# Kernel optimization log

Measured on AMD Instinct MI355X. Metric: run time of the kernel, lower is better.

Reference implementation:

```python
import jax, jax.numpy as jnp
import numpy as np

N, E, C, NB, NE, G = 20000, 320000, 64, 8, 4, 16
L2 = 9          # (max_ell+1)^2 with max_ell=2
RMAX = 5.0
HID = 16        # nonlinear readout hidden width


def setup_inputs():
    key = jax.random.key(0)
    ks = jax.random.split(key, 16)
    positions = jax.random.uniform(ks[0], (N, 3), dtype=jnp.float32) * 3.0
    elems = jax.random.randint(ks[1], (N,), 0, NE)
    node_attrs = jax.nn.one_hot(elems, NE, dtype=jnp.float32)
    edge_index = jax.random.randint(ks[2], (2, E), 0, N)
    batch = jnp.sort(jax.random.randint(ks[3], (N,), 0, G))
    shifts = jnp.zeros((E, 3), jnp.float32)
    atomic_energies = jnp.array([-1.0, -2.0, -3.0, -4.0], jnp.float32)
    sc = lambda k, shp, fan: jax.random.normal(k, shp, jnp.float32) / np.sqrt(fan).astype(np.float32)
    W_embed = sc(ks[4], (NE, C), NE)
    W_up = sc(ks[5], (2, C, C), C)
    W1 = sc(ks[6], (2, NB, 64), NB)
    W2 = sc(ks[7], (2, 64, C), 64)
    W_out = sc(ks[8], (2, C, C), C)
    W_skip = sc(ks[9], (2, NE, C), NE)
    w_read0 = sc(ks[10], (C,), C)
    W_r1 = sc(ks[11], (C, HID), C)
    w_r2 = sc(ks[12], (HID,), HID)
    return dict(positions=positions, node_attrs=node_attrs, shifts=shifts,
                atomic_energies=atomic_energies, W_embed=W_embed, W_up=W_up,
                W1=W1, W2=W2, W_out=W_out, W_skip=W_skip, w_read0=w_read0,
                W_r1=W_r1, w_r2=w_r2, edge_index=edge_index, batch=batch)


def _sph_harm_l2(u):
    # component-normalized real spherical harmonics up to l=2 on unit vectors
    x, y, z = u[:, 0], u[:, 1], u[:, 2]
    s3, s5, s15 = jnp.sqrt(3.0), jnp.sqrt(5.0), jnp.sqrt(15.0)
    return jnp.stack([jnp.ones_like(x),
                      s3 * x, s3 * y, s3 * z,
                      s15 * x * y, s15 * y * z, 0.5 * s5 * (3.0 * z * z - 1.0),
                      s15 * x * z, 0.5 * s15 * (x * x - y * y)], axis=-1)


def _radial(r):
    # Bessel radial basis with polynomial cutoff (p=6)
    n = jnp.arange(1, NB + 1, dtype=jnp.float32)
    rb = jnp.sqrt(2.0 / RMAX) * jnp.sin(n * jnp.pi * r[:, None] / RMAX) / r[:, None]
    u = r / RMAX
    fc = 1.0 - 28.0 * u**6 + 48.0 * u**7 - 21.0 * u**8
    fc = jnp.where(u < 1.0, fc, 0.0)
    return rb * fc[:, None]


def _energy_contributions(positions, node_attrs, shifts, atomic_energies,
                          W_embed, W_up, W1, W2, W_out, W_skip,
                          w_read0, W_r1, w_r2, edge_index, batch):
    snd, rcv = edge_index[0], edge_index[1]
    vec = positions[snd] - positions[rcv] + shifts                  # [E,3]
    r = jnp.sqrt(jnp.sum(vec * vec, axis=-1) + 1e-12)               # [E]
    Y = _sph_harm_l2(vec / r[:, None])                              # [E,L2]
    ef = _radial(r)                                                 # [E,NB]
    # E0: per-element reference energies, summed per graph
    e0 = jax.ops.segment_sum(node_attrs @ atomic_energies, batch, num_segments=G)
    h0 = node_attrs @ W_embed                                       # [N,C] scalar feats
    h = jnp.zeros((positions.shape[0], L2, C), h0.dtype).at[:, 0, :].set(h0)
    readouts = [lambda s: s @ w_read0,
                lambda s: jax.nn.silu(s @ W_r1) @ w_r2]             # linear / nonlinear
    energies = [e0]
    for i in range(2):
        hu = jnp.einsum('nlc,cd->nld', h, W_up[i])                  # channel mix
        R = jax.nn.silu(ef @ W1[i]) @ W2[i]                         # radial MLP [E,C]
        s = jnp.einsum('elc,el->ec', hu[snd], Y)                    # equivariant contraction
        m = Y[:, :, None] * (R * s)[:, None, :]                     # [E,L2,C] messages
        agg = jax.ops.segment_sum(m, rcv, num_segments=positions.shape[0])
        h = jnp.einsum('nlc,cd->nld', agg, W_out[i])
        h = h.at[:, 0, :].add(node_attrs @ W_skip[i])               # scalar skip connection
        node_en = readouts[i](h[:, 0, :])                           # [N]
        energies.append(jax.ops.segment_sum(node_en, batch, num_segments=G))
    return jnp.stack(energies, axis=-1)                             # [G, num_interactions+1]


def reference(positions, node_attrs, shifts, atomic_energies, W_embed, W_up,
              W1, W2, W_out, W_skip, w_read0, W_r1, w_r2, edge_index, batch):
    contributions = _energy_contributions(positions, node_attrs, shifts,
        atomic_energies, W_embed, W_up, W1, W2, W_out, W_skip,
        w_read0, W_r1, w_r2, edge_index, batch)
    total_energy = jnp.sum(contributions, axis=-1)                  # [G]
    forces = -jax.grad(lambda p: jnp.sum(_energy_contributions(p, node_attrs,
        shifts, atomic_energies, W_embed, W_up, W1, W2, W_out, W_skip,
        w_read0, W_r1, w_r2, edge_index, batch)))(positions)        # [N,3]
    return total_energy, contributions, forces
```

## Files before the change

kernel.cpp:

```cpp
#include <hip/hip_runtime.h>
#include <cmath>

constexpr int N_  = 20000;
constexpr int E_  = 320000;
constexpr int NE_ = 4;
constexpr int G_  = 16;
constexpr int CAP = 96;
constexpr int TAB = 4096;
constexpr float RMAXF = 5.0f;
constexpr float PI_F  = 3.14159265358979323846f;
constexpr float S3  = 1.7320508075688772f;
constexpr float S5  = 2.2360679774997896f;
constexpr float S15 = 3.8729833462074170f;
constexpr float KC_ = 0.6324555320336759f;

typedef unsigned short u16;
typedef unsigned int   u32;
typedef _Float16 f16;
typedef _Float16 f16x2 __attribute__((ext_vector_type(2)));

#define DEV static __device__ __forceinline__

__device__ float g_fallback[110000000];

DEV float sigmoidf_(float x){ return 1.0f/(1.0f+__expf(-x)); }

DEV float b2f(u16 u){ return __uint_as_float(((u32)u)<<16); }
DEV u16  f2b(float f){
  u32 x = __float_as_uint(f);
  return (u16)((x + 0x7FFFu + ((x>>16)&1u)) >> 16);
}
DEV u16  f2h(float f){ union{f16 h; u16 u;} v; v.h=(f16)f; return v.u; }
DEV float h2f(u16 u){ union{u16 u2; f16 h;} v; v.u2=u; return (float)v.h; }

DEV f16x2 u2h(u32 x){ union{u32 u; f16x2 h;} v; v.u=x; return v.h; }
DEV u32 h2u(f16x2 h){ union{u32 u; f16x2 h;} v; v.h=h; return v.u; }
DEV u32 pkh(float a, float b){ f16x2 h; h.x=(f16)a; h.y=(f16)b; return h2u(h); }

DEV void ld4(const float* __restrict__ p, float* d){
  float4 a = ((const float4*)p)[0];
  d[0]=a.x; d[1]=a.y; d[2]=a.z; d[3]=a.w;
}
DEV void ld4b(const u16* __restrict__ p, float* d){
  ushort4 a = *(const ushort4*)p;
  d[0]=b2f(a.x); d[1]=b2f(a.y); d[2]=b2f(a.z); d[3]=b2f(a.w);
}
DEV void ld4h(const u16* __restrict__ p, float* d){
  ushort4 a = *(const ushort4*)p;
  d[0]=h2f(a.x); d[1]=h2f(a.y); d[2]=h2f(a.z); d[3]=h2f(a.w);
}
DEV void st8b(u16* p, const float* d){
  uint4 v;
  v.x = (u32)f2b(d[0]) | ((u32)f2b(d[1])<<16);
  v.y = (u32)f2b(d[2]) | ((u32)f2b(d[3])<<16);
  v.z = (u32)f2b(d[4]) | ((u32)f2b(d[5])<<16);
  v.w = (u32)f2b(d[6]) | ((u32)f2b(d[7])<<16);
  *(uint4*)p = v;
}
DEV void st8h(u16* p, const float* d){
  uint4 v;
  v.x = pkh(d[0],d[1]); v.y = pkh(d[2],d[3]);
  v.z = pkh(d[4],d[5]); v.w = pkh(d[6],d[7]);
  *(uint4*)p = v;
}

__global__ void k_csr(const int* __restrict__ ei, int* __restrict__ cntR, int* __restrict__ cntS,
                      int* __restrict__ listR, int* __restrict__ listS){
  int e = blockIdx.x*256 + threadIdx.x;
  int s = ei[e], r = ei[E_+e];
  int p = atomicAdd(&cntR[r], 1); if (p < CAP) listR[r*CAP+p] = e;
  int q = atomicAdd(&cntS[s], 1); if (q < CAP) listS[s*CAP+q] = e;
}

__global__ void k_pre(const float* __restrict__ Wout0, const float* __restrict__ Wup1,
                      const float* __restrict__ Wskip0, const float* __restrict__ wread0,
                      float* __restrict__ WA, float* __restrict__ sa,
                      float* __restrict__ va, float* __restrict__ sv){
  int t = threadIdx.x;
  for (int idx=t; idx<4096; idx+=256){
    int c = idx>>6, d = idx&63;
    float acc=0.f;
    for (int m=0;m<64;++m) acc += Wout0[c*64+m]*Wup1[m*64+d];
    WA[idx]=acc;
  }
  {
    int k = t>>6, d = t&63;
    float acc=0.f;
    for (int m=0;m<64;++m) acc += Wskip0[k*64+m]*Wup1[m*64+d];
    sa[t]=acc;
  }
  if (t<64){
    float acc=0.f;
    for (int d=0;d<64;++d) acc += Wout0[t*64+d]*wread0[d];
    va[t]=acc;
  }
  if (t<4){
    float acc=0.f;
    for (int d=0;d<64;++d) acc += Wskip0[t*64+d]*wread0[d];
    sv[t]=acc;
  }
}

__global__ __launch_bounds__(256, 2)
void k_rtab(const float* __restrict__ W1g, const float* __restrict__ W2g,
            u16* __restrict__ tab){
  __shared__ float sW1[1024];
  __shared__ u32   sW2h[4096];
  __shared__ u32   sAh[32*36];
  int t = threadIdx.x;
  for (int i=t;i<1024;i+=256) sW1[i]=W1g[i];
  for (int i=t;i<4096;i+=256){
    int L = i>>11, rem = i&2047, kp = rem>>6, c = rem&63;
    sW2h[i] = pkh(W2g[L*4096 + (2*kp)*64 + c], W2g[L*4096 + (2*kp+1)*64 + c]);
  }
  __syncthreads();
  int wid=t>>6, lane=t&63, q=lane>>3, j=lane&7, c0=j*8;
  int slot = wid*8 + q;
  int knot = blockIdx.x*32 + slot;
  bool valid = (knot <= TAB);
  float rad = fmaxf((float)knot * (RMAXF/(float)TAB), 1e-6f);
  float inv = 1.0f/rad;
  float tt = rad*(1.0f/RMAXF);
  float fc = 0.0f, dfc = 0.0f;
  if (tt < 1.0f){
    float t2=tt*tt, t4=t2*t2, t5=t4*tt, t6=t5*tt, t7=t6*tt, t8=t7*tt;
    fc  = 1.0f - 28.0f*t6 + 48.0f*t7 - 21.0f*t8;
    dfc = (-168.0f*t5 + 336.0f*t6 - 168.0f*t7)*(1.0f/RMAXF);
  }
  float th = rad*(PI_F/RMAXF);
  float s1 = __sinf(th), c1 = __cosf(th);
  float base = KC_*inv*fc;
  float efv[8], gfv[8];
  {
    float sb = s1, cb = c1;
    #pragma unroll
    for (int b=0;b<8;++b){
      efv[b] = base*sb;
      float wb_ = (float)(b+1)*(PI_F/RMAXF);
      float rb  = KC_*sb*inv;
      float drb = KC_*(wb_*cb - sb*inv)*inv;
      gfv[b] = drb*fc + rb*dfc;
      float sn = sb*c1 + cb*s1;
      cb = cb*c1 - sb*s1;
      sb = sn;
    }
  }
  u32* myAh = sAh + slot*36;
  for (int L=0; L<2; ++L){
    const float* w1 = sW1 + L*512;
    const u32*  w2h = sW2h + L*2048;
    float zz[8]={0,0,0,0,0,0,0,0};
    float wgv[8]={0,0,0,0,0,0,0,0};
    #pragma unroll 4
    for (int b=0;b<8;++b){
      float efb = efv[b], gfb = gfv[b];
      const float4* w=(const float4*)(w1 + b*64 + c0);
      float4 wa=w[0], wb=w[1];
      zz[0]+=efb*wa.x; zz[1]+=efb*wa.y; zz[2]+=efb*wa.z; zz[3]+=efb*wa.w;
      zz[4]+=efb*wb.x; zz[5]+=efb*wb.y; zz[6]+=efb*wb.z; zz[7]+=efb*wb.w;
      wgv[0]+=gfb*wa.x; wgv[1]+=gfb*wa.y; wgv[2]+=gfb*wa.z; wgv[3]+=gfb*wa.w;
      wgv[4]+=gfb*wb.x; wgv[5]+=gfb*wb.y; wgv[6]+=gfb*wb.z; wgv[7]+=gfb*wb.w;
    }
    float a[8], dv[8];
    #pragma unroll
    for (int i=0;i<8;++i){
      float sg = sigmoidf_(zz[i]);
      a[i]  = zz[i]*sg;
      float sp = sg*(1.0f + zz[i]*(1.0f - sg));
      dv[i] = wgv[i]*sp;
    }
    {
      uint4 av;
      av.x = pkh(a[0],a[1]); av.y = pkh(a[2],a[3]);
      av.z = pkh(a[4],a[5]); av.w = pkh(a[6],a[7]);
      *(uint4*)(myAh + 4*j) = av;
    }
    {
      float r0=0.f,r1=0.f,r2=0.f,r3=0.f,r4=0.f,r5=0.f,r6=0.f,r7=0.f;
      #pragma unroll 2
      for (int kp4=0; kp4<8; ++kp4){
        uint4 dq = *(const uint4*)(myAh + 4*kp4);
        #pragma unroll
        for (int i=0;i<4;++i){
          u32 du = (i==0)?dq.x:(i==1)?dq.y:(i==2)?dq.z:dq.w;
          f16x2 dh = u2h(du);
          const u32* wrow = w2h + (4*kp4+i)*64 + c0;
          uint4 w0 = *(const uint4*)(wrow);
          uint4 w1v = *(const uint4*)(wrow+4);
          r0 = __builtin_amdgcn_fdot2(dh, u2h(w0.x),  r0, false);
          r1 = __builtin_amdgcn_fdot2(dh, u2h(w0.y),  r1, false);
          r2 = __builtin_amdgcn_fdot2(dh, u2h(w0.z),  r2, false);
          r3 = __builtin_amdgcn_fdot2(dh, u2h(w0.w),  r3, false);
          r4 = __builtin_amdgcn_fdot2(dh, u2h(w1v.x), r4, false);
          r5 = __builtin_amdgcn_fdot2(dh, u2h(w1v.y), r5, false);
          r6 = __builtin_amdgcn_fdot2(dh, u2h(w1v.z), r6, false);
          r7 = __builtin_amdgcn_fdot2(dh, u2h(w1v.w), r7, false);
        }
      }
      float racc[8] = {r0,r1,r2,r3,r4,r5,r6,r7};
      if (valid) st8h(tab + (size_t)knot*256 + L*64 + c0, racc);
    }
    {
      uint4 av;
      av.x = pkh(dv[0],dv[1]); av.y = pkh(dv[2],dv[3]);
      av.z = pkh(dv[4],dv[5]); av.w = pkh(dv[6],dv[7]);
      *(uint4*)(myAh + 4*j) = av;
    }
    {
      float r0=0.f,r1=0.f,r2=0.f,r3=0.f,r4=0.f,r5=0.f,r6=0.f,r7=0.f;
      #pragma unroll 2
      for (int kp4=0; kp4<8; ++kp4){
        uint4 dq = *(const uint4*)(myAh + 4*kp4);
        #pragma unroll
        for (int i=0;i<4;++i){
          u32 du = (i==0)?dq.x:(i==1)?dq.y:(i==2)?dq.z:dq.w;
          f16x2 dh = u2h(du);
          const u32* wrow = w2h + (4*kp4+i)*64 + c0;
          uint4 w0 = *(const uint4*)(wrow);
          uint4 w1v = *(const uint4*)(wrow+4);
          r0 = __builtin_amdgcn_fdot2(dh, u2h(w0.x),  r0, false);
          r1 = __builtin_amdgcn_fdot2(dh, u2h(w0.y),  r1, false);
          r2 = __builtin_amdgcn_fdot2(dh, u2h(w0.z),  r2, false);
          r3 = __builtin_amdgcn_fdot2(dh, u2h(w0.w),  r3, false);
          r4 = __builtin_amdgcn_fdot2(dh, u2h(w1v.x), r4, false);
          r5 = __builtin_amdgcn_fdot2(dh, u2h(w1v.y), r5, false);
          r6 = __builtin_amdgcn_fdot2(dh, u2h(w1v.z), r6, false);
          r7 = __builtin_amdgcn_fdot2(dh, u2h(w1v.w), r7, false);
        }
      }
      float qacc[8] = {r0,r1,r2,r3,r4,r5,r6,r7};
      if (valid) st8h(tab + (size_t)knot*256 + 128 + L*64 + c0, qacc);
    }
  }
}

__global__ void k_fwd_edge(const float* __restrict__ pos, const float* __restrict__ shifts,
                const int* __restrict__ ei, const u16* __restrict__ tab,
                float* __restrict__ Y, float* __restrict__ u3,
                float* __restrict__ irr,
                u16* __restrict__ R0, u16* __restrict__ R1,
                u16* __restrict__ q0, u16* __restrict__ q1){
  int t = threadIdx.x;
  int wid=t>>6, lane=t&63, q=lane>>3, j=lane&7, c0=j*8;
  int slot = wid*8 + q;
  int e = blockIdx.x*32 + slot;
  int snd = ei[e], rcv = ei[E_+e];
  float vx = pos[snd*3+0]-pos[rcv*3+0]+shifts[(size_t)e*3+0];
  float vy = pos[snd*3+1]-pos[rcv*3+1]+shifts[(size_t)e*3+1];
  float vz = pos[snd*3+2]-pos[rcv*3+2]+shifts[(size_t)e*3+2];
  float ss = vx*vx+vy*vy+vz*vz + 1e-12f;
  float rad = sqrtf(ss);
  float inv = 1.0f/rad;
  float x = vx*inv, y = vy*inv, z = vz*inv;
  if (j==0){
    irr[e]=inv;
    u3[(size_t)e*3+0]=x; u3[(size_t)e*3+1]=y; u3[(size_t)e*3+2]=z;
    float* Ye = Y + (size_t)e*9;
    Ye[0]=1.0f;
    Ye[1]=S3*x; Ye[2]=S3*y; Ye[3]=S3*z;
    Ye[4]=S15*x*y; Ye[5]=S15*y*z;
    Ye[6]=0.5f*S5*(3.0f*z*z-1.0f);
    Ye[7]=S15*x*z;
    Ye[8]=0.5f*S15*(x*x-y*y);
  }
  float vR0[8], vR1[8], vq0[8], vq1[8];
  if (rad < RMAXF){
    float xi = rad * ((float)TAB/RMAXF);
    int i0 = (int)xi; if (i0 > TAB-1) i0 = TAB-1;
    float f = xi - (float)i0;
    float g = 1.0f - f;
    const u16* ra = tab + (size_t)i0*256 + c0;
    const u16* rb = ra + 256;
    #pragma unroll
    for (int sec=0; sec<4; ++sec){
      ushort4 a0 = *(const ushort4*)(ra + sec*64);
      ushort4 a1 = *(const ushort4*)(ra + sec*64 + 4);
      ushort4 b0 = *(const ushort4*)(rb + sec*64);
      ushort4 b1 = *(const ushort4*)(rb + sec*64 + 4);
      float* dst = (sec==0)?vR0:(sec==1)?vR1:(sec==2)?vq0:vq1;
      dst[0]=h2f(a0.x)*g+h2f(b0.x)*f; dst[1]=h2f(a0.y)*g+h2f(b0.y)*f;
      dst[2]=h2f(a0.z)*g+h2f(b0.z)*f; dst[3]=h2f(a0.w)*g+h2f(b0.w)*f;
      dst[4]=h2f(a1.x)*g+h2f(b1.x)*f; dst[5]=h2f(a1.y)*g+h2f(b1.y)*f;
      dst[6]=h2f(a1.z)*g+h2f(b1.z)*f; dst[7]=h2f(a1.w)*g+h2f(b1.w)*f;
    }
  } else {
    #pragma unroll
    for (int i=0;i<8;++i){ vR0[i]=0.f; vR1[i]=0.f; vq0[i]=0.f; vq1[i]=0.f; }
  }
  st8b(R0 + (size_t)e*64 + c0, vR0);
  st8b(R1 + (size_t)e*64 + c0, vR1);
  st8h(q0 + (size_t)e*64 + c0, vq0);
  st8h(q1 + (size_t)e*64 + c0, vq1);
}

__global__ void k_e0(const float* __restrict__ attrs, const float* __restrict__ ae,
                     const int* __restrict__ batch, float* __restrict__ out){
  __shared__ float bins[G_];
  int t = threadIdx.x;
  if (t < G_) bins[t] = 0.f;
  __syncthreads();
  int n = blockIdx.x*256 + t;
  if (n < N_){
    float v = 0.f;
    #pragma unroll
    for (int k=0;k<NE_;++k) v += attrs[n*NE_+k]*ae[k];
    atomicAdd(&bins[batch[n]], v);
  }
  __syncthreads();
  if (t < G_){
    float b = bins[t];
    if (b != 0.f){
      atomicAdd(&out[t], b);
      atomicAdd(&out[G_ + t*3 + 0], b);
    }
  }
}

__global__ void k_wembup(const float* __restrict__ Wemb, const float* __restrict__ Wup0,
                         float* __restrict__ WembUp){
  int t = threadIdx.x; int k = t>>6, c = t&63;
  float acc = 0.f;
  for (int j=0;j<64;++j) acc += Wemb[k*64+j]*Wup0[j*64+c];
  WembUp[k*64+c] = acc;
}

__global__ void k_hu0(const float* __restrict__ attrs, const float* __restrict__ WembUp,
                      float* __restrict__ hu0){
  int i = blockIdx.x*256 + threadIdx.x;
  int n = i>>6, c = i&63;
  float acc = 0.f;
  #pragma unroll
  for (int k=0;k<NE_;++k) acc += attrs[n*NE_+k]*WembUp[k*64+c];
  hu0[i] = acc;
}

__global__ void k_agg0(const int* __restrict__ cntR, const int* __restrict__ listR,
                       const int* __restrict__ ei, const float* __restrict__ hu0,
                       const u16* __restrict__ R0, const float* __restrict__ Y,
                       float* __restrict__ agg0){
  int t = threadIdx.x; int n = blockIdx.x*4 + (t>>6); int c = t&63;
  float acc[9] = {0,0,0,0,0,0,0,0,0};
  int deg = min(cntR[n], CAP);
  #pragma unroll 2
  for (int j=0;j<deg;++j){
    int e = listR[n*CAP+j];
    int s = ei[e];
    float p = b2f(R0[(size_t)e*64+c])*hu0[(size_t)s*64+c];
    #pragma unroll
    for (int l=0;l<9;++l) acc[l] += Y[(size_t)e*9+l]*p;
  }
  #pragma unroll
  for (int l=0;l<9;++l) agg0[((size_t)n*9+l)*64+c] = acc[l];
}

__global__ void k_s1(const int* __restrict__ cntS, const int* __restrict__ listS,
                     const u16* __restrict__ hu1, const float* __restrict__ Y,
                     u16* __restrict__ s1){
  int t = threadIdx.x; int n = blockIdx.x*4 + (t>>6); int c = t&63;
  float hu[9];
  #pragma unroll
  for (int l=0;l<9;++l) hu[l] = b2f(hu1[((size_t)n*9+l)*64+c]);
  int deg = min(cntS[n], CAP);
  #pragma unroll 2
  for (int j=0;j<deg;++j){
    int e = listS[n*CAP+j];
    float acc = 0.f;
    #pragma unroll
    for (int l=0;l<9;++l) acc += hu[l]*Y[(size_t)e*9+l];
    s1[(size_t)e*64+c] = f2h(acc);
  }
}

__global__ void k_agg1(const int* __restrict__ cntR, const int* __restrict__ listR,
                       const u16* __restrict__ R1, const u16* __restrict__ s1,
                       float* __restrict__ agg1){
  int t = threadIdx.x; int n = blockIdx.x*4 + (t>>6); int c = t&63;
  float acc = 0.f;
  int deg = min(cntR[n], CAP);
  #pragma unroll 2
  for (int j=0;j<deg;++j){
    int e = listR[n*CAP+j];
    acc += b2f(R1[(size_t)e*64+c])*h2f(s1[(size_t)e*64+c]);
  }
  agg1[(size_t)n*64+c] = acc;
}

__global__ void k_dhu1(const int* __restrict__ cntS, const int* __restrict__ listS,
                       const int* __restrict__ ei, const u16* __restrict__ R1,
                       const float* __restrict__ ga1, const float* __restrict__ Y,
                       float* __restrict__ dhu1){
  int t = threadIdx.x; int n = blockIdx.x*4 + (t>>6); int c = t&63;
  float acc[9] = {0,0,0,0,0,0,0,0,0};
  int deg = min(cntS[n], CAP);
  #pragma unroll 2
  for (int j=0;j<deg;++j){
    int e = listS[n*CAP+j];
    int r = ei[E_+e];
    float ds = b2f(R1[(size_t)e*64+c])*ga1[(size_t)r*64+c];
    #pragma unroll
    for (int l=0;l<9;++l) acc[l] += Y[(size_t)e*9+l]*ds;
  }
  #pragma unroll
  for (int l=0;l<9;++l) dhu1[((size_t)n*9+l)*64+c] = acc[l];
}

template<bool TRANS, bool OUTB>
__global__ __launch_bounds__(256, 2)
void k_mm64(const float* __restrict__ in, const float* __restrict__ W,
            void* __restrict__ out, int rows, int lper,
            const float* __restrict__ attrs, const float* __restrict__ Wsk,
            const float* __restrict__ bias){
  __shared__ float sWT[64*68];
  __shared__ float sRow[4*68];
  int t = threadIdx.x;
  for (int i=t;i<4096;i+=256){
    int k=i&63, c=i>>6;
    sWT[c*68+k] = TRANS ? W[c*64+k] : W[k*64+c];
  }
  __syncthreads();
  int wid = t>>6, c = t&63;
  float wcol[64];
  {
    const float4* wp = (const float4*)(sWT + c*68);
    #pragma unroll
    for (int kk=0;kk<16;++kk){
      float4 w4 = wp[kk];
      wcol[4*kk+0]=w4.x; wcol[4*kk+1]=w4.y; wcol[4*kk+2]=w4.z; wcol[4*kk+3]=w4.w;
    }
  }
  float* myRow = sRow + wid*68;
  for (int it=0; it<8; ++it){
    int row = (blockIdx.x*8+it)*4 + wid;
    myRow[c] = in[(size_t)row*64+c];
    float acc = 0.f;
    #pragma unroll
    for (int kk=0;kk<16;++kk){
      float4 r4 = ((const float4*)myRow)[kk];
      acc += r4.x*wcol[4*kk+0] + r4.y*wcol[4*kk+1] + r4.z*wcol[4*kk+2] + r4.w*wcol[4*kk+3];
    }
    if (lper==1 || (row % 9)==0){
      int n = (lper==1) ? row : (row/9);
      if (attrs){
        #pragma unroll
        for (int k=0;k<NE_;++k) acc += attrs[n*NE_+k]*Wsk[k*64+c];
      }
      if (bias) acc += bias[c];
    }
    if (OUTB) ((u16*)out)[(size_t)row*64+c] = f2b(acc);
    else      ((float*)out)[(size_t)row*64+c] = acc;
  }
}

__global__ void k_read0(const float* __restrict__ agg0, const float* __restrict__ va,
                        const float* __restrict__ sv, const float* __restrict__ attrs,
                        const int* __restrict__ batch, float* __restrict__ out){
  __shared__ float bins[G_];
  int t = threadIdx.x;
  if (t < G_) bins[t] = 0.f;
  __syncthreads();
  int lane = t & 63, wid = t >> 6;
  int grp = lane >> 3, j = lane & 7;
  int n = blockIdx.x*32 + wid*8 + grp;
  const float* hp = agg0 + (size_t)n*576 + j*8;
  const float* wp = va + j*8;
  float4 h0 = ((const float4*)hp)[0], h4 = ((const float4*)hp)[1];
  float4 w0v = ((const float4*)wp)[0], w4v = ((const float4*)wp)[1];
  float v = h0.x*w0v.x + h0.y*w0v.y + h0.z*w0v.z + h0.w*w0v.w
          + h4.x*w4v.x + h4.y*w4v.y + h4.z*w4v.z + h4.w*w4v.w;
  v += __shfl_xor(v,1,64); v += __shfl_xor(v,2,64); v += __shfl_xor(v,4,64);
  if (j==0){
    v += attrs[n*NE_+0]*sv[0] + attrs[n*NE_+1]*sv[1]
       + attrs[n*NE_+2]*sv[2] + attrs[n*NE_+3]*sv[3];
    atomicAdd(&bins[batch[n]], v);
  }
  __syncthreads();
  if (t < G_){
    float b = bins[t];
    if (b != 0.f){
      atomicAdd(&out[t], b);
      atomicAdd(&out[G_ + t*3 + 1], b);
    }
  }
}

__global__ void k_read1(const float* __restrict__ h2, const float* __restrict__ Wr1,
                        const float* __restrict__ wr2, const int* __restrict__ batch,
                        float* __restrict__ spz, float* __restrict__ out){
  __shared__ float sW[64*16];
  __shared__ float sA[256];
  __shared__ float bins[G_];
  int t = threadIdx.x;
  for (int i=t;i<1024;i+=256) sW[i]=Wr1[i];
  if (t < G_) bins[t] = 0.f;
  __syncthreads();
  int n = blockIdx.x*16 + (t>>4); int j = t&15;
  float z = 0.f;
  #pragma unroll 16
  for (int c=0;c<64;++c) z += h2[(size_t)n*64+c]*sW[c*16+j];
  float sg = sigmoidf_(z);
  float a  = z*sg;
  float sp = sg*(1.0f + z*(1.0f - sg));
  float w2v = wr2[j];
  spz[n*16+j] = sp*w2v;
  sA[t] = a*w2v;
  __syncthreads();
  if (j==0){
    float s = 0.f;
    #pragma unroll
    for (int k=0;k<16;++k) s += sA[t+k];
    atomicAdd(&bins[batch[n]], s);
  }
  __syncthreads();
  if (t < G_){
    float b = bins[t];
    if (b != 0.f){
      atomicAdd(&out[t], b);
      atomicAdd(&out[G_ + t*3 + 2], b);
    }
  }
}

__global__ void k_dh2(const float* __restrict__ Wr1, const float* __restrict__ spz,
                      float* __restrict__ dh2){
  int i = blockIdx.x*256 + threadIdx.x;
  int n = i>>6, c = i&63;
  float acc = 0.f;
  #pragma unroll
  for (int j=0;j<16;++j) acc += Wr1[c*16+j]*spz[n*16+j];
  dh2[i] = acc;
}

__global__ __launch_bounds__(256, 4)
void k_bedge_all(const int* __restrict__ ei, const float* __restrict__ Y,
             const float* __restrict__ u3, const float* __restrict__ irr,
             const u16* __restrict__ R0b, const u16* __restrict__ R1b,
             const float* __restrict__ ga1, const u16* __restrict__ ga0,
             const float* __restrict__ hu0, const u16* __restrict__ hu1,
             const u16* __restrict__ q0b, const u16* __restrict__ q1b,
             float* __restrict__ gF){
  int t = threadIdx.x;
  int wid=t>>6, lane=t&63, q=lane>>4, j=lane&15, c0=j*4;
  int slot = wid*4+q;
  int e = blockIdx.x*16 + slot;
  int snd = ei[e], rcv = ei[E_+e];
  float Yl[9];
  #pragma unroll
  for (int l=0;l<9;++l) Yl[l] = Y[(size_t)e*9+l];
  ushort4 huv1[9];
  #pragma unroll
  for (int l=0;l<9;++l) huv1[l] = *(const ushort4*)(hu1 + ((size_t)snd*9 + l)*64 + c0);
  ushort4 gv0[9];
  #pragma unroll
  for (int l=0;l<9;++l) gv0[l] = *(const ushort4*)(ga0 + ((size_t)rcv*9 + l)*64 + c0);
  float T1[4];  ld4(ga1 + (size_t)rcv*64 + c0, T1);
  float hu0v[4]; ld4(hu0 + (size_t)snd*64 + c0, hu0v);
  float R1v[4]; ld4b(R1b + (size_t)e*64 + c0, R1v);
  float R0v[4]; ld4b(R0b + (size_t)e*64 + c0, R0v);
  float q1v[4]; ld4h(q1b + (size_t)e*64 + c0, q1v);
  float q0v[4]; ld4h(q0b + (size_t)e*64 + c0, q0v);
  float dyp[9];
  float dR1[4];
  {
    float ds1[4], sA[4];
    #pragma unroll
    for (int i=0;i<4;++i){ ds1[i]=R1v[i]*T1[i]; sA[i]=0.f; }
    #pragma unroll
    for (int l=0;l<9;++l){
      float h0v=b2f(huv1[l].x), h1v=b2f(huv1[l].y), h2v=b2f(huv1[l].z), h3v=b2f(huv1[l].w);
      float Ylv = Yl[l];
      sA[0]+=h0v*Ylv; sA[1]+=h1v*Ylv; sA[2]+=h2v*Ylv; sA[3]+=h3v*Ylv;
      dyp[l] = ds1[0]*h0v + ds1[1]*h1v + ds1[2]*h2v + ds1[3]*h3v;
    }
    #pragma unroll
    for (int i=0;i<4;++i) dR1[i]=sA[i]*T1[i];
  }
  float dR0[4];
  {
    float P[4], T0[4];
    #pragma unroll
    for (int i=0;i<4;++i){ P[i]=R0v[i]*hu0v[i]; T0[i]=0.f; }
    #pragma unroll
    for (int l=0;l<9;++l){
      float g0=b2f(gv0[l].x), g1=b2f(gv0[l].y), g2=b2f(gv0[l].z), g3=b2f(gv0[l].w);
      float Ylv = Yl[l];
      T0[0]+=g0*Ylv; T0[1]+=g1*Ylv; T0[2]+=g2*Ylv; T0[3]+=g3*Ylv;
      dyp[l] += g0*P[0] + g1*P[1] + g2*P[2] + g3*P[3];
    }
    #pragma unroll
    for (int i=0;i<4;++i) dR0[i]=hu0v[i]*T0[i];
  }
  float dy[9];
  #pragma unroll
  for (int l=1;l<9;++l){
    float v=dyp[l];
    v += __shfl_xor(v,1,64); v += __shfl_xor(v,2,64);
    v += __shfl_xor(v,4,64); v += __shfl_xor(v,8,64);
    dy[l]=v;
  }
  float dr = q1v[0]*dR1[0]+q1v[1]*dR1[1]+q1v[2]*dR1[2]+q1v[3]*dR1[3]
           + q0v[0]*dR0[0]+q0v[1]*dR0[1]+q0v[2]*dR0[2]+q0v[3]*dR0[3];
  dr += __shfl_xor(dr,1,64); dr += __shfl_xor(dr,2,64);
  dr += __shfl_xor(dr,4,64); dr += __shfl_xor(dr,8,64);
  float x = u3[(size_t)e*3+0], y = u3[(size_t)e*3+1], zz = u3[(size_t)e*3+2];
  float invr = irr[e];
  float dux = S3*dy[1] + S15*(y*dy[4] + zz*dy[7] + x*dy[8]);
  float duy = S3*dy[2] + S15*(x*dy[4] + zz*dy[5] - y*dy[8]);
  float duz = S3*dy[3] + S15*(y*dy[5] + x*dy[7]) + 3.0f*S5*zz*dy[6];
  float udot = x*dux + y*duy + zz*duz;
  float gx = dr*x + invr*(dux - x*udot);
  float gy = dr*y + invr*(duy - y*udot);
  float gz = dr*zz + invr*(duz - zz*udot);
  if (j==0){
    float* gp2 = gF + (size_t)e*3;
    gp2[0]=gx; gp2[1]=gy; gp2[2]=gz;
  }
}

__global__ void k_fsum(const int* __restrict__ cnts, const int* __restrict__ lists,
                       const float* __restrict__ gF, float* __restrict__ F){
  int t = threadIdx.x;
  int lane = t & 63, wid = t >> 6;
  int sub = lane >> 3, j = lane & 7;
  int n = blockIdx.x*32 + wid*8 + sub;
  const int* cntR = cnts;       const int* cntS = cnts + N_;
  const int* listR = lists;     const int* listS = lists + (size_t)N_*CAP;
  float fx=0.f, fy=0.f, fz=0.f;
  int dRn = min(cntR[n], CAP);
  for (int k=j;k<dRn;k+=8){
    int e = listR[n*CAP+k];
    fx += gF[(size_t)e*3+0]; fy += gF[(size_t)e*3+1]; fz += gF[(size_t)e*3+2];
  }
  int dSn = min(cntS[n], CAP);
  for (int k=j;k<dSn;k+=8){
    int e = listS[n*CAP+k];
    fx -= gF[(size_t)e*3+0]; fy -= gF[(size_t)e*3+1]; fz -= gF[(size_t)e*3+2];
  }
  fx += __shfl_xor(fx,1,64); fy += __shfl_xor(fy,1,64); fz += __shfl_xor(fz,1,64);
  fx += __shfl_xor(fx,2,64); fy += __shfl_xor(fy,2,64); fz += __shfl_xor(fz,2,64);
  fx += __shfl_xor(fx,4,64); fy += __shfl_xor(fy,4,64); fz += __shfl_xor(fz,4,64);
  if (j==0){
    F[n*3+0]=fx; F[n*3+1]=fy; F[n*3+2]=fz;
  }
}

extern "C" void kernel_launch(void* const* d_in, const int* in_sizes, int n_in,
                              void* d_out, int out_size, void* d_ws, size_t ws_size,
                              hipStream_t stream){
  (void)in_sizes; (void)n_in;
  const float* pos    = (const float*)d_in[0];
  const float* attrs  = (const float*)d_in[1];
  const float* shifts = (const float*)d_in[2];
  const float* ae     = (const float*)d_in[3];
  const float* Wemb   = (const float*)d_in[4];
  const float* Wup    = (const float*)d_in[5];
  const float* W1     = (const float*)d_in[6];
  const float* W2     = (const float*)d_in[7];
  const float* Wout   = (const float*)d_in[8];
  const float* Wskip  = (const float*)d_in[9];
  const float* wread0 = (const float*)d_in[10];
  const float* Wr1    = (const float*)d_in[11];
  const float* wr2    = (const float*)d_in[12];
  const int*   ei     = (const int*)d_in[13];
  const int*   batch  = (const int*)d_in[14];
  float* out = (float*)d_out;

  const size_t NEED = 430000000;
  char* base;
  if (ws_size >= NEED){
    base = (char*)d_ws;
  } else {
    void* p = nullptr;
    hipGetSymbolAddress(&p, HIP_SYMBOL(g_fallback));
    base = (char*)p;
  }
  size_t off = 0;
  auto alloc = [&](size_t bytes)->char*{
    char* p = base + off;
    off += ((bytes + 255)/256)*256;
    return p;
  };
  float* Y    = (float*)alloc((size_t)E_*9*4);
  float* u3   = (float*)alloc((size_t)E_*3*4);
  float* irr  = (float*)alloc((size_t)E_*4);
  u16*   R0   = (u16*)  alloc((size_t)E_*64*2);
  u16*   R1   = (u16*)  alloc((size_t)E_*64*2);
  u16*   q0   = (u16*)  alloc((size_t)E_*64*2);
  u16*   q1   = (u16*)  alloc((size_t)E_*64*2);
  u16*   s1b  = (u16*)  alloc((size_t)E_*64*2);
  float* gF   = (float*)alloc((size_t)E_*3*4);
  u16*   tab  = (u16*)  alloc((size_t)(TAB+1)*256*2);
  float* hu0  = (float*)alloc((size_t)N_*64*4);
  u16*   hu1  = (u16*)  alloc((size_t)N_*9*64*2);
  float* agg0 = (float*)alloc((size_t)N_*9*64*4);
  float* agg1 = (float*)alloc((size_t)N_*64*4);
  float* h2   = (float*)alloc((size_t)N_*64*4);
  float* spz  = (float*)alloc((size_t)N_*16*4);
  float* dh2  = (float*)alloc((size_t)N_*64*4);
  float* ga1  = (float*)alloc((size_t)N_*64*4);
  u16*   ga0  = (u16*)  alloc((size_t)N_*9*64*2);
  float* WembUp = (float*)alloc(256*4);
  float* WA   = (float*)alloc(4096*4);
  float* sa   = (float*)alloc(256*4);
  float* va   = (float*)alloc(64*4);
  float* sv   = (float*)alloc(4*4);
  int* cnts  = (int*)alloc((size_t)2*N_*4);
  int* lists = (int*)alloc((size_t)2*N_*CAP*4);
  int* cntR = cnts;          int* cntS = cnts + N_;
  int* listR = lists;        int* listS = lists + (size_t)N_*CAP;
  float* dhu1 = agg0;
  float* F = out + G_ + G_*3;

  hipMemsetAsync(d_out, 0, (size_t)out_size*sizeof(float), stream);
  hipMemsetAsync(cnts, 0, (size_t)2*N_*sizeof(int), stream);

  k_csr     <<<E_/256, 256, 0, stream>>>(ei, cntR, cntS, listR, listS);
  k_rtab    <<<(TAB+1+31)/32, 256, 0, stream>>>(W1, W2, tab);
  k_fwd_edge<<<E_/32, 256, 0, stream>>>(pos, shifts, ei, tab, Y, u3, irr, R0, R1, q0, q1);
  k_wembup  <<<1, 256, 0, stream>>>(Wemb, Wup, WembUp);
  k_pre     <<<1, 256, 0, stream>>>(Wout, Wup + 4096, Wskip, wread0, WA, sa, va, sv);
  k_e0      <<<(N_+255)/256, 256, 0, stream>>>(attrs, ae, batch, out);
  k_hu0     <<<N_*64/256, 256, 0, stream>>>(attrs, WembUp, hu0);
  k_agg0    <<<N_/4, 256, 0, stream>>>(cntR, listR, ei, hu0, R0, Y, agg0);
  k_mm64<false,true><<<N_*9/32, 256, 0, stream>>>(agg0, WA, hu1, N_*9, 9, attrs, sa, nullptr);
  k_read0   <<<N_/32, 256, 0, stream>>>(agg0, va, sv, attrs, batch, out);
  k_s1      <<<N_/4, 256, 0, stream>>>(cntS, listS, hu1, Y, s1b);
  k_agg1    <<<N_/4, 256, 0, stream>>>(cntR, listR, R1, s1b, agg1);
  k_mm64<false,false><<<N_/32, 256, 0, stream>>>(agg1, Wout + 4096, h2, N_, 1, attrs, Wskip + 256, nullptr);
  k_read1   <<<N_/16, 256, 0, stream>>>(h2, Wr1, wr2, batch, spz, out);

  k_dh2     <<<N_*64/256, 256, 0, stream>>>(Wr1, spz, dh2);
  k_mm64<true,false><<<N_/32, 256, 0, stream>>>(dh2, Wout + 4096, ga1, N_, 1, nullptr, nullptr, nullptr);
  k_dhu1    <<<N_/4, 256, 0, stream>>>(cntS, listS, ei, R1, ga1, Y, dhu1);
  k_mm64<true,true><<<N_*9/32, 256, 0, stream>>>(dhu1, WA, ga0, N_*9, 9, nullptr, nullptr, va);
  k_bedge_all<<<E_/16, 256, 0, stream>>>(ei, Y, u3, irr, R0, R1, ga1, ga0, hu0, hu1, q0, q1, gF);
  k_fsum    <<<N_/32, 256, 0, stream>>>(cnts, lists, gF, F);
}
```

Before: 792.7 us.

## Sort edges by receiver into CSR order so per-edge arrays are contiguous

Replaces the capped receiver lists with a count, scan and permute pass that renumbers edges in receiver-sorted order. All per-edge buffers (Y, R0, R1, s1, gF) are now indexed by the sorted position, so receiver-side aggregations read contiguous rows instead of gathering through an index list. The sender list now stores sorted positions. This adds two extra launches, a single-block scan and three permutation arrays, and the sender-side kernels still gather.

```diff
diff --git a/kernel.cpp b/kernel.cpp
--- a/kernel.cpp
+++ b/kernel.cpp
@@ -64,12 +64,39 @@
   *(uint4*)p = v;
 }
 
-__global__ void k_csr(const int* __restrict__ ei, int* __restrict__ cntR, int* __restrict__ cntS,
-                      int* __restrict__ listR, int* __restrict__ listS){
+__global__ void k_cnt(const int* __restrict__ ei, int* __restrict__ cntR){
+  int e = blockIdx.x*256 + threadIdx.x;
+  atomicAdd(&cntR[ei[E_+e]], 1);
+}
+
+__global__ void k_scan(const int* __restrict__ cntR, int* __restrict__ offR){
+  __shared__ int part[256];
+  int t = threadIdx.x;
+  constexpr int CH = (N_+255)/256;
+  int base = t*CH;
+  int s=0;
+  for (int i=0;i<CH;++i){ int idx=base+i; if(idx<N_) s+=cntR[idx]; }
+  part[t]=s; __syncthreads();
+  for (int d=1; d<256; d<<=1){
+    int v = (t>=d)? part[t-d] : 0;
+    __syncthreads();
+    part[t]+=v;
+    __syncthreads();
+  }
+  int run = (t==0)?0:part[t-1];
+  for (int i=0;i<CH;++i){ int idx=base+i; if(idx<N_){ offR[idx]=run; run+=cntR[idx]; } }
+  if (t==255) offR[N_]=run;
+}
+
+__global__ void k_perm(const int* __restrict__ ei, const int* __restrict__ offR,
+                       int* __restrict__ cntR2, int* __restrict__ cntS,
+                       int* __restrict__ pe, int* __restrict__ pSnd, int* __restrict__ pRcv,
+                       int* __restrict__ listS){
   int e = blockIdx.x*256 + threadIdx.x;
   int s = ei[e], r = ei[E_+e];
-  int p = atomicAdd(&cntR[r], 1); if (p < CAP) listR[r*CAP+p] = e;
-  int q = atomicAdd(&cntS[s], 1); if (q < CAP) listS[s*CAP+q] = e;
+  int p = offR[r] + atomicAdd(&cntR2[r], 1);
+  pe[p] = e; pSnd[p] = s; pRcv[p] = r;
+  int q = atomicAdd(&cntS[s], 1); if (q < CAP) listS[s*CAP+q] = p;
 }
 
 __global__ void k_pre(const float* __restrict__ Wout0, const float* __restrict__ Wup1,
@@ -235,7 +262,8 @@
 }
 
 __global__ void k_fwd_edge(const float* __restrict__ pos, const float* __restrict__ shifts,
-                const int* __restrict__ ei, const u16* __restrict__ tab,
+                const int* __restrict__ pe, const int* __restrict__ pSnd,
+                const int* __restrict__ pRcv, const u16* __restrict__ tab,
                 float* __restrict__ Y, float* __restrict__ u3,
                 float* __restrict__ irr,
                 u16* __restrict__ R0, u16* __restrict__ R1,
@@ -244,10 +272,11 @@
   int wid=t>>6, lane=t&63, q=lane>>3, j=lane&7, c0=j*8;
   int slot = wid*8 + q;
   int e = blockIdx.x*32 + slot;
-  int snd = ei[e], rcv = ei[E_+e];
-  float vx = pos[snd*3+0]-pos[rcv*3+0]+shifts[(size_t)e*3+0];
-  float vy = pos[snd*3+1]-pos[rcv*3+1]+shifts[(size_t)e*3+1];
-  float vz = pos[snd*3+2]-pos[rcv*3+2]+shifts[(size_t)e*3+2];
+  int eo  = pe[e];
+  int snd = pSnd[e], rcv = pRcv[e];
+  float vx = pos[snd*3+0]-pos[rcv*3+0]+shifts[(size_t)eo*3+0];
+  float vy = pos[snd*3+1]-pos[rcv*3+1]+shifts[(size_t)eo*3+1];
+  float vz = pos[snd*3+2]-pos[rcv*3+2]+shifts[(size_t)eo*3+2];
   float ss = vx*vx+vy*vy+vz*vz + 1e-12f;
   float rad = sqrtf(ss);
   float inv = 1.0f/rad;
@@ -334,20 +363,18 @@
   hu0[i] = acc;
 }
 
-__global__ void k_agg0(const int* __restrict__ cntR, const int* __restrict__ listR,
-                       const int* __restrict__ ei, const float* __restrict__ hu0,
+__global__ void k_agg0(const int* __restrict__ offR, const int* __restrict__ pSnd,
+                       const float* __restrict__ hu0,
                        const u16* __restrict__ R0, const float* __restrict__ Y,
                        float* __restrict__ agg0){
   int t = threadIdx.x; int n = blockIdx.x*4 + (t>>6); int c = t&63;
   float acc[9] = {0,0,0,0,0,0,0,0,0};
-  int deg = min(cntR[n], CAP);
-  #pragma unroll 2
-  for (int j=0;j<deg;++j){
-    int e = listR[n*CAP+j];
-    int s = ei[e];
-    float p = b2f(R0[(size_t)e*64+c])*hu0[(size_t)s*64+c];
-    #pragma unroll
-    for (int l=0;l<9;++l) acc[l] += Y[(size_t)e*9+l]*p;
+  int p0 = offR[n], p1 = offR[n+1];
+  for (int p=p0;p<p1;++p){
+    int s = pSnd[p];
+    float v = b2f(R0[(size_t)p*64+c])*hu0[(size_t)s*64+c];
+    #pragma unroll
+    for (int l=0;l<9;++l) acc[l] += Y[(size_t)p*9+l]*v;
   }
   #pragma unroll
   for (int l=0;l<9;++l) agg0[((size_t)n*9+l)*64+c] = acc[l];
@@ -363,30 +390,28 @@
   int deg = min(cntS[n], CAP);
   #pragma unroll 2
   for (int j=0;j<deg;++j){
-    int e = listS[n*CAP+j];
+    int p = listS[n*CAP+j];
     float acc = 0.f;
     #pragma unroll
-    for (int l=0;l<9;++l) acc += hu[l]*Y[(size_t)e*9+l];
-    s1[(size_t)e*64+c] = f2h(acc);
-  }
-}
-
-__global__ void k_agg1(const int* __restrict__ cntR, const int* __restrict__ listR,
+    for (int l=0;l<9;++l) acc += hu[l]*Y[(size_t)p*9+l];
+    s1[(size_t)p*64+c] = f2h(acc);
+  }
+}
+
+__global__ void k_agg1(const int* __restrict__ offR,
                        const u16* __restrict__ R1, const u16* __restrict__ s1,
                        float* __restrict__ agg1){
   int t = threadIdx.x; int n = blockIdx.x*4 + (t>>6); int c = t&63;
   float acc = 0.f;
-  int deg = min(cntR[n], CAP);
-  #pragma unroll 2
-  for (int j=0;j<deg;++j){
-    int e = listR[n*CAP+j];
-    acc += b2f(R1[(size_t)e*64+c])*h2f(s1[(size_t)e*64+c]);
+  int p0 = offR[n], p1 = offR[n+1];
+  for (int p=p0;p<p1;++p){
+    acc += b2f(R1[(size_t)p*64+c])*h2f(s1[(size_t)p*64+c]);
   }
   agg1[(size_t)n*64+c] = acc;
 }
 
 __global__ void k_dhu1(const int* __restrict__ cntS, const int* __restrict__ listS,
-                       const int* __restrict__ ei, const u16* __restrict__ R1,
+                       const int* __restrict__ pRcv, const u16* __restrict__ R1,
                        const float* __restrict__ ga1, const float* __restrict__ Y,
                        float* __restrict__ dhu1){
   int t = threadIdx.x; int n = blockIdx.x*4 + (t>>6); int c = t&63;
@@ -394,11 +419,11 @@
   int deg = min(cntS[n], CAP);
   #pragma unroll 2
   for (int j=0;j<deg;++j){
-    int e = listS[n*CAP+j];
-    int r = ei[E_+e];
-    float ds = b2f(R1[(size_t)e*64+c])*ga1[(size_t)r*64+c];
-    #pragma unroll
-    for (int l=0;l<9;++l) acc[l] += Y[(size_t)e*9+l]*ds;
+    int p = listS[n*CAP+j];
+    int r = pRcv[p];
+    float ds = b2f(R1[(size_t)p*64+c])*ga1[(size_t)r*64+c];
+    #pragma unroll
+    for (int l=0;l<9;++l) acc[l] += Y[(size_t)p*9+l]*ds;
   }
   #pragma unroll
   for (int l=0;l<9;++l) dhu1[((size_t)n*9+l)*64+c] = acc[l];
@@ -531,7 +556,8 @@
 }
 
 __global__ __launch_bounds__(256, 4)
-void k_bedge_all(const int* __restrict__ ei, const float* __restrict__ Y,
+void k_bedge_all(const int* __restrict__ pSnd, const int* __restrict__ pRcv,
+             const float* __restrict__ Y,
              const float* __restrict__ u3, const float* __restrict__ irr,
              const u16* __restrict__ R0b, const u16* __restrict__ R1b,
              const float* __restrict__ ga1, const u16* __restrict__ ga0,
@@ -542,7 +568,7 @@
   int wid=t>>6, lane=t&63, q=lane>>4, j=lane&15, c0=j*4;
   int slot = wid*4+q;
   int e = blockIdx.x*16 + slot;
-  int snd = ei[e], rcv = ei[E_+e];
+  int snd = pSnd[e], rcv = pRcv[e];
   float Yl[9];
   #pragma unroll
   for (int l=0;l<9;++l) Yl[l] = Y[(size_t)e*9+l];
@@ -616,24 +642,22 @@
   }
 }
 
-__global__ void k_fsum(const int* __restrict__ cnts, const int* __restrict__ lists,
+__global__ void k_fsum(const int* __restrict__ offR, const int* __restrict__ cntS,
+                       const int* __restrict__ listS,
                        const float* __restrict__ gF, float* __restrict__ F){
   int t = threadIdx.x;
   int lane = t & 63, wid = t >> 6;
   int sub = lane >> 3, j = lane & 7;
   int n = blockIdx.x*32 + wid*8 + sub;
-  const int* cntR = cnts;       const int* cntS = cnts + N_;
-  const int* listR = lists;     const int* listS = lists + (size_t)N_*CAP;
   float fx=0.f, fy=0.f, fz=0.f;
-  int dRn = min(cntR[n], CAP);
-  for (int k=j;k<dRn;k+=8){
-    int e = listR[n*CAP+k];
-    fx += gF[(size_t)e*3+0]; fy += gF[(size_t)e*3+1]; fz += gF[(size_t)e*3+2];
+  int p0 = offR[n], p1 = offR[n+1];
+  for (int p=p0+j; p<p1; p+=8){
+    fx += gF[(size_t)p*3+0]; fy += gF[(size_t)p*3+1]; fz += gF[(size_t)p*3+2];
   }
   int dSn = min(cntS[n], CAP);
   for (int k=j;k<dSn;k+=8){
-    int e = listS[n*CAP+k];
-    fx -= gF[(size_t)e*3+0]; fy -= gF[(size_t)e*3+1]; fz -= gF[(size_t)e*3+2];
+    int p = listS[n*CAP+k];
+    fx -= gF[(size_t)p*3+0]; fy -= gF[(size_t)p*3+1]; fz -= gF[(size_t)p*3+2];
   }
   fx += __shfl_xor(fx,1,64); fy += __shfl_xor(fy,1,64); fz += __shfl_xor(fz,1,64);
   fx += __shfl_xor(fx,2,64); fy += __shfl_xor(fy,2,64); fz += __shfl_xor(fz,2,64);
@@ -703,35 +727,41 @@
   float* sa   = (float*)alloc(256*4);
   float* va   = (float*)alloc(64*4);
   float* sv   = (float*)alloc(4*4);
-  int* cnts  = (int*)alloc((size_t)2*N_*4);
-  int* lists = (int*)alloc((size_t)2*N_*CAP*4);
-  int* cntR = cnts;          int* cntS = cnts + N_;
-  int* listR = lists;        int* listS = lists + (size_t)N_*CAP;
+  int* cnts  = (int*)alloc((size_t)3*N_*4);
+  int* offR  = (int*)alloc((size_t)(N_+1)*4);
+  int* pe    = (int*)alloc((size_t)E_*4);
+  int* pSnd  = (int*)alloc((size_t)E_*4);
+  int* pRcv  = (int*)alloc((size_t)E_*4);
+  int* listS = (int*)alloc((size_t)N_*CAP*4);
+  int* cntR = cnts;  int* cntS = cnts + N_;  int* cntR2 = cnts + 2*N_;
   float* dhu1 = agg0;
   float* F = out + G_ + G_*3;
 
   hipMemsetAsync(d_out, 0, (size_t)out_size*sizeof(float), stream);
-  hipMemsetAsync(cnts, 0, (size_t)2*N_*sizeof(int), stream);
-
-  k_csr     <<<E_/256, 256, 0, stream>>>(ei, cntR, cntS, listR, listS);
+  hipMemsetAsync(cnts, 0, (size_t)3*N_*sizeof(int), stream);
+
+  k_cnt     <<<E_/256, 256, 0, stream>>>(ei, cntR);
+  k_scan    <<<1, 256, 0, stream>>>(cntR, offR);
+  k_perm    <<<E_/256, 256, 0, stream>>>(ei, offR, cntR2, cntS, pe, pSnd, pRcv, listS);
+
   k_rtab    <<<(TAB+1+31)/32, 256, 0, stream>>>(W1, W2, tab);
-  k_fwd_edge<<<E_/32, 256, 0, stream>>>(pos, shifts, ei, tab, Y, u3, irr, R0, R1, q0, q1);
+  k_fwd_edge<<<E_/32, 256, 0, stream>>>(pos, shifts, pe, pSnd, pRcv, tab, Y, u3, irr, R0, R1, q0, q1);
   k_wembup  <<<1, 256, 0, stream>>>(Wemb, Wup, WembUp);
   k_pre     <<<1, 256, 0, stream>>>(Wout, Wup + 4096, Wskip, wread0, WA, sa, va, sv);
   k_e0      <<<(N_+255)/256, 256, 0, stream>>>(attrs, ae, batch, out);
   k_hu0     <<<N_*64/256, 256, 0, stream>>>(attrs, WembUp, hu0);
-  k_agg0    <<<N_/4, 256, 0, stream>>>(cntR, listR, ei, hu0, R0, Y, agg0);
+  k_agg0    <<<N_/4, 256, 0, stream>>>(offR, pSnd, hu0, R0, Y, agg0);
   k_mm64<false,true><<<N_*9/32, 256, 0, stream>>>(agg0, WA, hu1, N_*9, 9, attrs, sa, nullptr);
   k_read0   <<<N_/32, 256, 0, stream>>>(agg0, va, sv, attrs, batch, out);
   k_s1      <<<N_/4, 256, 0, stream>>>(cntS, listS, hu1, Y, s1b);
-  k_agg1    <<<N_/4, 256, 0, stream>>>(cntR, listR, R1, s1b, agg1);
+  k_agg1    <<<N_/4, 256, 0, stream>>>(offR, R1, s1b, agg1);
   k_mm64<false,false><<<N_/32, 256, 0, stream>>>(agg1, Wout + 4096, h2, N_, 1, attrs, Wskip + 256, nullptr);
   k_read1   <<<N_/16, 256, 0, stream>>>(h2, Wr1, wr2, batch, spz, out);
 
   k_dh2     <<<N_*64/256, 256, 0, stream>>>(Wr1, spz, dh2);
   k_mm64<true,false><<<N_/32, 256, 0, stream>>>(dh2, Wout + 4096, ga1, N_, 1, nullptr, nullptr, nullptr);
-  k_dhu1    <<<N_/4, 256, 0, stream>>>(cntS, listS, ei, R1, ga1, Y, dhu1);
+  k_dhu1    <<<N_/4, 256, 0, stream>>>(cntS, listS, pRcv, R1, ga1, Y, dhu1);
   k_mm64<true,true><<<N_*9/32, 256, 0, stream>>>(dhu1, WA, ga0, N_*9, 9, nullptr, nullptr, va);
-  k_bedge_all<<<E_/16, 256, 0, stream>>>(ei, Y, u3, irr, R0, R1, ga1, ga0, hu0, hu1, q0, q1, gF);
-  k_fsum    <<<N_/32, 256, 0, stream>>>(cnts, lists, gF, F);
-}
+  k_bedge_all<<<E_/16, 256, 0, stream>>>(pSnd, pRcv, Y, u3, irr, R0, R1, ga1, ga0, hu0, hu1, q0, q1, gF);
+  k_fsum    <<<N_/32, 256, 0, stream>>>(offR, cntS, listS, gF, F);
+}
```

Result: faster. 771.3 us (-2.7%).
